# Performance work log

Hardware: AMD Instinct MI355X
Metric: run time of the kernel (lower is better)

## Reference

```python
import jax, jax.numpy as jnp
import numpy as np

B, N, L, D = 128, 1024, 512, 64


def setup_inputs() -> dict:
    key = jax.random.key(0)
    k1, k2 = jax.random.split(key)
    text_outputs = jax.random.normal(k1, (B, N, D), dtype=jnp.float32)
    image_outputs = jax.random.normal(k2, (B, L, D), dtype=jnp.float32)
    rng = np.random.RandomState(0)
    ntok = rng.randint(N // 4, N + 1, size=B)
    nreg = rng.randint(L // 4, L + 1, size=B)
    text_mask = (np.arange(N)[None, :] < ntok[:, None]).astype(np.float32)
    image_mask = (np.arange(L)[None, :] < nreg[:, None]).astype(np.float32)
    # impostor indices (torch code samples these with np.random inside forward;
    # here they are fixed constants for determinism), guaranteed != own index
    I_imp = rng.randint(0, B, size=B)
    S_imp = rng.randint(0, B, size=B)
    ar = np.arange(B)
    I_imp = np.where(I_imp == ar, (I_imp + 1) % B, I_imp).astype(np.int32)
    S_imp = np.where(S_imp == ar, (S_imp + 1) % B, S_imp).astype(np.int32)
    return {
        "text_outputs": text_outputs,
        "image_outputs": image_outputs,
        "text_mask": jnp.asarray(text_mask),
        "image_mask": jnp.asarray(image_mask),
        "I_imp_idx": jnp.asarray(I_imp),
        "S_imp_idx": jnp.asarray(S_imp),
    }


def _mean_max_sim(T, I, tmask, imask):
    # T: (N, D) tokens, I: (L, D) regions; masks select the ragged valid prefix.
    M = jnp.einsum('nd,ld->nl', T, I)                       # matchmap (N, L)
    neg = jnp.finfo(M.dtype).min
    mx = jnp.max(jnp.where(imask[None, :] > 0, M, neg), axis=1)  # max over regions
    return jnp.sum(mx * tmask) / jnp.sum(tmask)             # mean over valid tokens


def reference(text_outputs, image_outputs, text_mask, image_mask, I_imp_idx, S_imp_idx, margin=1.0):
    sim = jax.vmap(_mean_max_sim)
    anchor = sim(text_outputs, image_outputs, text_mask, image_mask)            # (B,)
    Simpsim = sim(text_outputs[S_imp_idx], image_outputs, text_mask[S_imp_idx], image_mask)
    Iimpsim = sim(text_outputs, image_outputs[I_imp_idx], text_mask, image_mask[I_imp_idx])
    # scalar per-sample hinge: term added only when margin+imp-anchor > 0 == relu
    per_sample = jax.nn.relu(margin + Iimpsim - anchor) + jax.nn.relu(margin + Simpsim - anchor)
    loss = jnp.sum(per_sample) / text_outputs.shape[0]
    return loss[None]  # torch returns shape (1,)
```

## Files before the change

kernel.cpp:

```cpp
#include <hip/hip_runtime.h>
#include <hip/hip_bf16.h>

#define B 128
#define N 1024
#define L 512
#define D 64

typedef float f32x4 __attribute__((ext_vector_type(4)));
typedef short bf16x8 __attribute__((ext_vector_type(8)));

__device__ inline bf16x8 cvt8(float4 f0, float4 f1) {
    union { __hip_bfloat162 h2[4]; bf16x8 v; } u;
    u.h2[0] = __float22bfloat162_rn(make_float2(f0.x, f0.y));
    u.h2[1] = __float22bfloat162_rn(make_float2(f0.z, f0.w));
    u.h2[2] = __float22bfloat162_rn(make_float2(f1.x, f1.y));
    u.h2[3] = __float22bfloat162_rn(make_float2(f1.z, f1.w));
    return u.v;
}

__device__ __forceinline__ void gload16(const void* g, void* l) {
    __builtin_amdgcn_global_load_lds(
        (const __attribute__((address_space(1))) void*)g,
        (__attribute__((address_space(3))) void*)l, 16, 0, 0);
}

__global__ __launch_bounds__(256) void count_kernel(
        const float* __restrict__ tmask, const float* __restrict__ imask,
        int* __restrict__ counts) {
    int b = blockIdx.x, tid = threadIdx.x;
    int w = tid >> 6, lane = tid & 63;
    float ts = 0.f, is = 0.f;
    const float* tm = tmask + (size_t)b * N;
#pragma unroll
    for (int i = 0; i < N / 256; ++i) ts += tm[tid + i * 256];
    const float* im = imask + (size_t)b * L;
#pragma unroll
    for (int i = 0; i < L / 256; ++i) is += im[tid + i * 256];
    for (int off = 32; off; off >>= 1) {
        ts += __shfl_down(ts, off);
        is += __shfl_down(is, off);
    }
    __shared__ float red[8];
    if (lane == 0) { red[w] = ts; red[4 + w] = is; }
    __syncthreads();
    if (tid == 0) counts[b]     = (int)(red[0] + red[1] + red[2] + red[3] + 0.5f);
    if (tid == 1) counts[B + b] = (int)(red[4] + red[5] + red[6] + red[7] + 0.5f);
}

__global__ __launch_bounds__(256, 3) void sim_kernel(
        const float* __restrict__ T, const float* __restrict__ I,
        const int* __restrict__ counts,
        const int* __restrict__ Iimp, const int* __restrict__ Simp,
        float* __restrict__ partials) {
    int blk = blockIdx.x;
    int chunk = blk & 3;
    int bs = blk >> 2;
    int b = bs & (B - 1);
    int s = bs >> 7;
    int Tb = b, Ib = b;
    if (s == 1) Tb = Simp[b];
    else if (s == 2) Ib = Iimp[b];

    int tid = threadIdx.x;
    int w = tid >> 6;
    int lane = tid & 63;
    int q = lane >> 4;
    int c = lane & 15;

    int ntok = counts[Tb];
    int nreg = counts[B + Ib];

    int tok0 = chunk << 8;
    if (chunk != 0 && tok0 >= ntok) {
        if (tid == 0) partials[blk] = 0.f;
        return;
    }

    __shared__ float ldsI[3][4096];
    __shared__ float red[4];

    int wt0 = tok0 + w * 64;
    bf16x8 afrag[4][2];
#pragma unroll
    for (int tt = 0; tt < 4; ++tt) {
        const float* trow = T + ((size_t)Tb * N + wt0 + tt * 16 + c) * D;
#pragma unroll
        for (int h = 0; h < 2; ++h) {
            const float4* p = (const float4*)(trow + h * 32 + q * 8);
            afrag[tt][h] = cvt8(p[0], p[1]);
        }
    }

    float mx[4][4];
#pragma unroll
    for (int tt = 0; tt < 4; ++tt)
#pragma unroll
        for (int i = 0; i < 4; ++i) mx[tt][i] = -3.0e38f;

    int rloc[4], foff[4];
#pragma unroll
    for (int j = 0; j < 4; ++j) {
        int ci = tid + j * 256;
        int fh = ci >> 7, idx = ci & 127, half = idx >> 6, ln2 = idx & 63;
        rloc[j] = (fh >> 1) * 16 + (ln2 & 15);
        foff[j] = (fh & 1) * 32 + (ln2 >> 4) * 8 + half * 4;
    }
    const float* Ibase = I + (size_t)Ib * L * D;
    int nchunks = (nreg + 63) >> 6;
    int nregm1 = nreg - 1;

    auto stage = [&](int k) {
        float* buf = &ldsI[k % 3][0];
        int rbase = k << 6;
#pragma unroll
        for (int j = 0; j < 4; ++j) {
            int r = rbase + rloc[j];
            if (r > nregm1) r = nregm1;
            gload16(Ibase + (size_t)r * D + foff[j], buf + (tid + j * 256) * 4);
        }
    };

    asm volatile("s_waitcnt vmcnt(0)" ::: "memory");
    stage(0);
    stage(1);
    asm volatile("s_waitcnt vmcnt(4)" ::: "memory");
    __builtin_amdgcn_s_barrier();

    for (int k = 0; k < nchunks; ++k) {
        if (k + 2 < nchunks) stage(k + 2);

        const char* base = (const char*)&ldsI[k % 3][0] + (size_t)lane * 16;
#pragma unroll
        for (int rt = 0; rt < 4; ++rt) {
            float4 e0 = *(const float4*)(base + (rt * 2 + 0) * 2048);
            float4 e1 = *(const float4*)(base + (rt * 2 + 0) * 2048 + 1024);
            float4 e2 = *(const float4*)(base + (rt * 2 + 1) * 2048);
            float4 e3 = *(const float4*)(base + (rt * 2 + 1) * 2048 + 1024);
            bf16x8 b0 = cvt8(e0, e1);
            bf16x8 b1 = cvt8(e2, e3);
#pragma unroll
            for (int tt = 0; tt < 4; ++tt) {
                f32x4 acc = {0.f, 0.f, 0.f, 0.f};
                acc = __builtin_amdgcn_mfma_f32_16x16x32_bf16(afrag[tt][0], b0, acc, 0, 0, 0);
                acc = __builtin_amdgcn_mfma_f32_16x16x32_bf16(afrag[tt][1], b1, acc, 0, 0, 0);
#pragma unroll
                for (int i = 0; i < 4; ++i) mx[tt][i] = fmaxf(mx[tt][i], acc[i]);
            }
        }

        if (k + 1 < nchunks) {
            if (k + 2 < nchunks)
                asm volatile("s_waitcnt vmcnt(4) lgkmcnt(0)" ::: "memory");
            else
                asm volatile("s_waitcnt vmcnt(0) lgkmcnt(0)" ::: "memory");
            __builtin_amdgcn_s_barrier();
        }
    }

#pragma unroll
    for (int m = 1; m < 16; m <<= 1) {
#pragma unroll
        for (int tt = 0; tt < 4; ++tt)
#pragma unroll
            for (int i = 0; i < 4; ++i)
                mx[tt][i] = fmaxf(mx[tt][i], __shfl_xor(mx[tt][i], m));
    }

    float bsum = 0.f;
    if (c == 0) {
#pragma unroll
        for (int tt = 0; tt < 4; ++tt)
#pragma unroll
            for (int i = 0; i < 4; ++i) {
                int row = wt0 + tt * 16 + q * 4 + i;
                if (row < ntok) bsum += mx[tt][i];
            }
    }
    for (int off = 32; off; off >>= 1) bsum += __shfl_down(bsum, off);
    if (lane == 0) red[w] = bsum;
    __syncthreads();
    if (tid == 0)
        partials[blk] = (red[0] + red[1] + red[2] + red[3]) / (float)ntok;
}

__global__ void loss_kernel(const float* __restrict__ partials,
                            float* __restrict__ out) {
    int tid = threadIdx.x;
    __shared__ float simsL[384];
    __shared__ float w6[6];
    const float4* p4 = (const float4*)partials;
    float4 v = p4[tid];
    simsL[tid] = v.x + v.y + v.z + v.w;
    __syncthreads();
    float per = 0.f;
    if (tid < B) {
        float anc  = simsL[tid];
        float simp = simsL[B + tid];
        float iimp = simsL[2 * B + tid];
        per = fmaxf(1.f + iimp - anc, 0.f) + fmaxf(1.f + simp - anc, 0.f);
    }
    for (int off = 32; off; off >>= 1) per += __shfl_down(per, off);
    if ((tid & 63) == 0) w6[tid >> 6] = per;
    __syncthreads();
    if (tid == 0)
        out[0] = (w6[0] + w6[1] + w6[2] + w6[3] + w6[4] + w6[5]) / (float)B;
}

extern "C" void kernel_launch(void* const* d_in, const int* in_sizes, int n_in,
                              void* d_out, int out_size, void* d_ws, size_t ws_size,
                              hipStream_t stream) {
    const float* T     = (const float*)d_in[0];
    const float* I     = (const float*)d_in[1];
    const float* tmask = (const float*)d_in[2];
    const float* imask = (const float*)d_in[3];
    const int*   Iimp  = (const int*)d_in[4];
    const int*   Simp  = (const int*)d_in[5];
    int*   counts   = (int*)d_ws;
    float* partials = (float*)d_ws + 256;

    count_kernel<<<B, 256, 0, stream>>>(tmask, imask, counts);
    sim_kernel<<<3 * B * 4, 256, 0, stream>>>(T, I, counts, Iimp, Simp, partials);
    loss_kernel<<<1, 384, 0, stream>>>(partials, (float*)d_out);
}
```

Before: 129.9 us.

## Pre-convert image features to bf16 once and stream bf16 tiles in sim kernel

Adds a prep kernel that computes mask counts and also converts the whole image tensor to bf16 in workspace. The similarity kernel then stages bf16 tiles directly into LDS, which halves global and LDS traffic per chunk and drops the per-chunk fp32-to-bf16 conversion, raising occupancy to 4 blocks. This costs an extra full pass over the image tensor (read fp32, write bf16) and falls back to the old path when the workspace is too small.

```diff
diff --git a/kernel.cpp b/kernel.cpp
--- a/kernel.cpp
+++ b/kernel.cpp
@@ -24,6 +24,173 @@
         (__attribute__((address_space(3))) void*)l, 16, 0, 0);
 }
 
+__global__ __launch_bounds__(256) void prep_kernel(
+        const float* __restrict__ tmask, const float* __restrict__ imask,
+        const float* __restrict__ I,
+        int* __restrict__ counts, unsigned short* __restrict__ Ibf) {
+    int blk = blockIdx.x, tid = threadIdx.x;
+    if (blk < B) {
+        int b = blk;
+        int w = tid >> 6, lane = tid & 63;
+        float ts = 0.f, is = 0.f;
+        const float* tm = tmask + (size_t)b * N;
+#pragma unroll
+        for (int i = 0; i < N / 256; ++i) ts += tm[tid + i * 256];
+        const float* im = imask + (size_t)b * L;
+#pragma unroll
+        for (int i = 0; i < L / 256; ++i) is += im[tid + i * 256];
+        for (int off = 32; off; off >>= 1) {
+            ts += __shfl_down(ts, off);
+            is += __shfl_down(is, off);
+        }
+        __shared__ float red[8];
+        if (lane == 0) { red[w] = ts; red[4 + w] = is; }
+        __syncthreads();
+        if (tid == 0) counts[b]     = (int)(red[0] + red[1] + red[2] + red[3] + 0.5f);
+        if (tid == 1) counts[B + b] = (int)(red[4] + red[5] + red[6] + red[7] + 0.5f);
+    } else {
+        int t = (blk - B) * 256 + tid;
+#pragma unroll
+        for (int j = 0; j < 4; ++j) {
+            size_t ci = (size_t)t + (size_t)j * 131072;
+            const float4* p = (const float4*)(I + ci * 8);
+            *(bf16x8*)(Ibf + ci * 8) = cvt8(p[0], p[1]);
+        }
+    }
+}
+
+__global__ __launch_bounds__(256, 4) void sim_kernel_bf16(
+        const float* __restrict__ T, const unsigned short* __restrict__ Ibf,
+        const int* __restrict__ counts,
+        const int* __restrict__ Iimp, const int* __restrict__ Simp,
+        float* __restrict__ partials) {
+    int blk = blockIdx.x;
+    int chunk = blk & 3;
+    int bs = blk >> 2;
+    int b = bs & (B - 1);
+    int s = bs >> 7;
+    int Tb = b, Ib = b;
+    if (s == 1) Tb = Simp[b];
+    else if (s == 2) Ib = Iimp[b];
+
+    int tid = threadIdx.x;
+    int w = tid >> 6;
+    int lane = tid & 63;
+    int q = lane >> 4;
+    int c = lane & 15;
+
+    int ntok = counts[Tb];
+    int nreg = counts[B + Ib];
+
+    int tok0 = chunk << 8;
+    if (chunk != 0 && tok0 >= ntok) {
+        if (tid == 0) partials[blk] = 0.f;
+        return;
+    }
+
+    __shared__ unsigned short ldsI[3][4096];
+    __shared__ float red[4];
+
+    int wt0 = tok0 + w * 64;
+    bf16x8 afrag[4][2];
+#pragma unroll
+    for (int tt = 0; tt < 4; ++tt) {
+        const float* trow = T + ((size_t)Tb * N + wt0 + tt * 16 + c) * D;
+#pragma unroll
+        for (int h = 0; h < 2; ++h) {
+            const float4* p = (const float4*)(trow + h * 32 + q * 8);
+            afrag[tt][h] = cvt8(p[0], p[1]);
+        }
+    }
+
+    float mx[4][4];
+#pragma unroll
+    for (int tt = 0; tt < 4; ++tt)
+#pragma unroll
+        for (int i = 0; i < 4; ++i) mx[tt][i] = -3.0e38f;
+
+    int rloc[2], eoff[2];
+#pragma unroll
+    for (int j = 0; j < 2; ++j) {
+        int ci = tid + j * 256;
+        int g = ci >> 6, ln = ci & 63;
+        rloc[j] = (g >> 1) * 16 + (ln & 15);
+        eoff[j] = (g & 1) * 32 + (ln >> 4) * 8;
+    }
+    const unsigned short* Ibase = Ibf + (size_t)Ib * L * D;
+    int nchunks = (nreg + 63) >> 6;
+    int nregm1 = nreg - 1;
+
+    auto stage = [&](int k) {
+        unsigned short* buf = &ldsI[k % 3][0];
+        int rbase = k << 6;
+#pragma unroll
+        for (int j = 0; j < 2; ++j) {
+            int r = rbase + rloc[j];
+            if (r > nregm1) r = nregm1;
+            gload16(Ibase + (size_t)r * D + eoff[j], buf + (size_t)(tid + j * 256) * 8);
+        }
+    };
+
+    asm volatile("s_waitcnt vmcnt(0)" ::: "memory");
+    stage(0);
+    stage(1);
+    asm volatile("s_waitcnt vmcnt(2)" ::: "memory");
+    __builtin_amdgcn_s_barrier();
+
+    for (int k = 0; k < nchunks; ++k) {
+        if (k + 2 < nchunks) stage(k + 2);
+
+        const char* base = (const char*)&ldsI[k % 3][0] + (size_t)lane * 16;
+#pragma unroll
+        for (int rt = 0; rt < 4; ++rt) {
+            bf16x8 b0 = *(const bf16x8*)(base + (rt * 2 + 0) * 1024);
+            bf16x8 b1 = *(const bf16x8*)(base + (rt * 2 + 1) * 1024);
+#pragma unroll
+            for (int tt = 0; tt < 4; ++tt) {
+                f32x4 acc = {0.f, 0.f, 0.f, 0.f};
+                acc = __builtin_amdgcn_mfma_f32_16x16x32_bf16(afrag[tt][0], b0, acc, 0, 0, 0);
+                acc = __builtin_amdgcn_mfma_f32_16x16x32_bf16(afrag[tt][1], b1, acc, 0, 0, 0);
+#pragma unroll
+                for (int i = 0; i < 4; ++i) mx[tt][i] = fmaxf(mx[tt][i], acc[i]);
+            }
+        }
+
+        if (k + 1 < nchunks) {
+            if (k + 2 < nchunks)
+                asm volatile("s_waitcnt vmcnt(2) lgkmcnt(0)" ::: "memory");
+            else
+                asm volatile("s_waitcnt vmcnt(0) lgkmcnt(0)" ::: "memory");
+            __builtin_amdgcn_s_barrier();
+        }
+    }
+
+#pragma unroll
+    for (int m = 1; m < 16; m <<= 1) {
+#pragma unroll
+        for (int tt = 0; tt < 4; ++tt)
+#pragma unroll
+            for (int i = 0; i < 4; ++i)
+                mx[tt][i] = fmaxf(mx[tt][i], __shfl_xor(mx[tt][i], m));
+    }
+
+    float bsum = 0.f;
+    if (c == 0) {
+#pragma unroll
+        for (int tt = 0; tt < 4; ++tt)
+#pragma unroll
+            for (int i = 0; i < 4; ++i) {
+                int row = wt0 + tt * 16 + q * 4 + i;
+                if (row < ntok) bsum += mx[tt][i];
+            }
+    }
+    for (int off = 32; off; off >>= 1) bsum += __shfl_down(bsum, off);
+    if (lane == 0) red[w] = bsum;
+    __syncthreads();
+    if (tid == 0)
+        partials[blk] = (red[0] + red[1] + red[2] + red[3]) / (float)ntok;
+}
+
 __global__ __launch_bounds__(256) void count_kernel(
         const float* __restrict__ tmask, const float* __restrict__ imask,
         int* __restrict__ counts) {
@@ -47,7 +214,7 @@
     if (tid == 1) counts[B + b] = (int)(red[4] + red[5] + red[6] + red[7] + 0.5f);
 }
 
-__global__ __launch_bounds__(256, 3) void sim_kernel(
+__global__ __launch_bounds__(256, 3) void sim_kernel_f32(
         const float* __restrict__ T, const float* __restrict__ I,
         const int* __restrict__ counts,
         const int* __restrict__ Iimp, const int* __restrict__ Simp,
@@ -216,9 +383,16 @@
     const int*   Iimp  = (const int*)d_in[4];
     const int*   Simp  = (const int*)d_in[5];
     int*   counts   = (int*)d_ws;
-    float* partials = (float*)d_ws + 256;
-
-    count_kernel<<<B, 256, 0, stream>>>(tmask, imask, counts);
-    sim_kernel<<<3 * B * 4, 256, 0, stream>>>(T, I, counts, Iimp, Simp, partials);
+    float* partials = (float*)((char*)d_ws + 1024);
+    size_t need_bf16 = 7168 + (size_t)B * L * D * sizeof(unsigned short);
+
+    if (ws_size >= need_bf16) {
+        unsigned short* Ibf = (unsigned short*)((char*)d_ws + 7168);
+        prep_kernel<<<B + 512, 256, 0, stream>>>(tmask, imask, I, counts, Ibf);
+        sim_kernel_bf16<<<3 * B * 4, 256, 0, stream>>>(T, Ibf, counts, Iimp, Simp, partials);
+    } else {
+        count_kernel<<<B, 256, 0, stream>>>(tmask, imask, counts);
+        sim_kernel_f32<<<3 * B * 4, 256, 0, stream>>>(T, I, counts, Iimp, Simp, partials);
+    }
     loss_kernel<<<1, 384, 0, stream>>>(partials, (float*)d_out);
 }
```

Measured after the change: 122.1 us. 1.06x faster.
